# Kernel optimization log

Measured on AMD Instinct MI355X. Metric: run time of the kernel, lower is better.

## Reference

```python
import jax, jax.numpy as jnp
import numpy as np

B, T, N, F_IN = 8, 12, 20000, 2
H, HORIZON, K = 64, 12, 2
E = 320000


def setup_inputs() -> dict:
    key = jax.random.key(0)
    ks = jax.random.split(key, 12)
    s = 0.05
    return dict(
        x=jax.random.normal(ks[0], (B, T, N, F_IN), jnp.float32),
        edge_index=jax.random.randint(ks[1], (2, E), 0, N),
        edge_weight=jax.random.uniform(ks[2], (E,), jnp.float32),
        enc_w=jax.random.normal(ks[3], (F_IN, H), jnp.float32) * s,
        enc_b=jnp.zeros((H,), jnp.float32),
        node_emb=jax.random.normal(ks[4], (N, H), jnp.float32) * s,
        w_ih=jax.random.normal(ks[5], (3 * H, H), jnp.float32) * s,
        w_hh=jax.random.normal(ks[6], (3 * H, H), jnp.float32) * s,
        b_ih=jnp.zeros((3 * H,), jnp.float32),
        b_hh=jnp.zeros((3 * H,), jnp.float32),
        filt_w=jax.random.normal(ks[7], (H * (2 * K + 1), H), jnp.float32) * s,
        filt_b=jnp.zeros((H,), jnp.float32),
        dec_w=jax.random.normal(ks[8], (H, F_IN * HORIZON), jnp.float32) * s,
        dec_b=jnp.zeros((F_IN * HORIZON,), jnp.float32),
    )


def _gru_last(x_seq, w_ih, w_hh, b_ih, b_hh):
    # x_seq: [BN, T, H] -> last hidden state [BN, H] (torch GRU gate math)
    bn = x_seq.shape[0]
    h0 = jnp.zeros((bn, H), x_seq.dtype)
    # precompute input-side gates: [T, BN, 3H]
    xg = jnp.swapaxes(jnp.einsum('bth,gh->btg', x_seq, w_ih) + b_ih, 0, 1)

    def step(h, xg_t):
        hg = h @ w_hh.T + b_hh
        xr, xz, xn = jnp.split(xg_t, 3, axis=-1)
        hr, hz, hn = jnp.split(hg, 3, axis=-1)
        r = jax.nn.sigmoid(xr + hr)
        z = jax.nn.sigmoid(xz + hz)
        n = jnp.tanh(xn + r * hn)
        return (1.0 - z) * n + z * h, None

    h_last, _ = jax.lax.scan(step, h0, xg)
    return h_last


def _norm_weights(w, idx):
    # normalize edge weights by in-degree of aggregation index (tsl normalize)
    deg = jax.ops.segment_sum(w, idx, num_segments=N)
    inv = jnp.where(deg > 0, 1.0 / deg, 0.0)
    return w * inv[idx]


def _propagate(h, src, tgt, w):
    # h: [B, N, H]; message x_j * w aggregated (sum) at target
    msg = h[:, src, :] * w[None, :, None]           # [B, E, H]
    return jnp.zeros_like(h).at[:, tgt, :].add(msg)


def reference(x, edge_index, edge_weight, enc_w, enc_b, node_emb,
              w_ih, w_hh, b_ih, b_hh, filt_w, filt_b, dec_w, dec_b):
    b, t, n, _ = x.shape
    # linear encode + node embeddings
    x_emb = x @ enc_w + enc_b + node_emb[None, None]          # [B, T, N, H]
    # per-node GRU over time
    x_rnn = jnp.transpose(x_emb, (0, 2, 1, 3)).reshape(b * n, t, H)
    h = _gru_last(x_rnn, w_ih, w_hh, b_ih, b_hh).reshape(b, n, H)
    # diffusion graph conv: root + k hops forward + k hops backward
    src, tgt = edge_index[0], edge_index[1]
    w_fwd = _norm_weights(edge_weight, tgt)
    w_bwd = _norm_weights(edge_weight, src)
    outs = [h]
    for s_idx, t_idx, w in ((src, tgt, w_fwd), (tgt, src, w_bwd)):
        hs = h
        for _ in range(K):
            hs = _propagate(hs, s_idx, t_idx, w)
            outs.append(hs)
    z = jnp.concatenate(outs, axis=-1) @ filt_w + filt_b      # [B, N, H]
    # decode and rearrange 'b n (t f) -> b t n f'
    x_out = z @ dec_w + dec_b                                 # [B, N, HORIZON*F_IN]
    x_hor = x_out.reshape(b, n, HORIZON, F_IN)
    return jnp.transpose(x_hor, (0, 2, 1, 3))                 # [B, HORIZON, N, F_IN]
```

## Files before the change

kernel.cpp:

```cpp
#include <hip/hip_runtime.h>

#define NN 20000
#define NE 320000
#define NB 8
#define NT 12

typedef unsigned int u32;
typedef short bf16x8 __attribute__((ext_vector_type(8)));
typedef float f32x4 __attribute__((ext_vector_type(4)));
typedef u32   u32x2 __attribute__((ext_vector_type(2)));

union U8 { u32 u[4]; bf16x8 v; };

__device__ __forceinline__ float bcast(float v, int k) {
  return __int_as_float(__builtin_amdgcn_readlane(__float_as_int(v), k));
}
__device__ __forceinline__ u32 cvt_pk_bf16(float a, float b) {
  u32 r;
  asm("v_cvt_pk_bf16_f32 %0, %1, %2" : "=v"(r) : "v"(a), "v"(b));
  return r;
}
__device__ __forceinline__ float rcpf(float x) {
  float r;
  asm("v_rcp_f32 %0, %1" : "=v"(r) : "v"(x));
  return r;
}
__device__ __forceinline__ unsigned short f2bf(float f) {
  u32 u = __float_as_uint(f);
  u32 r = (u + 0x7FFFu + ((u >> 16) & 1u)) >> 16;
  return (unsigned short)r;
}
__device__ __forceinline__ float bf2f(unsigned short s) {
  return __uint_as_float(((u32)s) << 16);
}

__global__ void deg_kernel(const int* __restrict__ ei, const float* __restrict__ ew,
                           float* __restrict__ wsum_f, float* __restrict__ wsum_b,
                           int* __restrict__ cnt_f, int* __restrict__ cnt_b) {
  int e = blockIdx.x * 256 + threadIdx.x;
  if (e >= NE) return;
  int s = ei[e], t = ei[NE + e];
  float wv = ew[e];
  atomicAdd(&wsum_f[t], wv);
  atomicAdd(&cnt_f[t], 1);
  atomicAdd(&wsum_b[s], wv);
  atomicAdd(&cnt_b[s], 1);
}

__global__ __launch_bounds__(1024) void scan_kernel(
    const int* __restrict__ cnt_f, const int* __restrict__ cnt_b,
    int* __restrict__ rp_f, int* __restrict__ rp_b,
    int* __restrict__ cur_f, int* __restrict__ cur_b) {
  __shared__ int sm[1024];
  const int tid = threadIdx.x;
  for (int pass = 0; pass < 2; ++pass) {
    const int* cnt = pass ? cnt_b : cnt_f;
    int* rp  = pass ? rp_b  : rp_f;
    int* cur = pass ? cur_b : cur_f;
    const int base = tid * 20;
    int4 c4[5];
    int s = 0;
    if (base < NN) {
      const int4* cp = (const int4*)(cnt + base);
#pragma unroll
      for (int j = 0; j < 5; j++) c4[j] = cp[j];
#pragma unroll
      for (int j = 0; j < 5; j++) s += c4[j].x + c4[j].y + c4[j].z + c4[j].w;
    }
    __syncthreads();
    sm[tid] = s;
    __syncthreads();
    for (int off = 1; off < 1024; off <<= 1) {
      int v = (tid >= off) ? sm[tid - off] : 0;
      __syncthreads();
      sm[tid] += v;
      __syncthreads();
    }
    if (base < NN) {
      int run = sm[tid] - s;
      int4* rp4  = (int4*)(rp + base);
      int4* cur4 = (int4*)(cur + base);
#pragma unroll
      for (int j = 0; j < 5; j++) {
        int4 o;
        o.x = run; run += c4[j].x;
        o.y = run; run += c4[j].y;
        o.z = run; run += c4[j].z;
        o.w = run; run += c4[j].w;
        rp4[j] = o;
        cur4[j] = o;
      }
    }
    if (tid == 1023) rp[NN] = sm[1023];
  }
}

__global__ void fill_kernel(const int* __restrict__ ei, const float* __restrict__ ew,
                            const float* __restrict__ wsum_f, const float* __restrict__ wsum_b,
                            int* __restrict__ cur_f, int* __restrict__ cur_b,
                            int* __restrict__ col_f, float* __restrict__ wn_f,
                            int* __restrict__ col_b, float* __restrict__ wn_b) {
  int e = blockIdx.x * 256 + threadIdx.x;
  if (e >= NE) return;
  int s = ei[e], t = ei[NE + e];
  float wv = ew[e];
  int slot = atomicAdd(&cur_f[t], 1);
  float w1 = wsum_f[t];
  col_f[slot] = s;
  wn_f[slot] = (w1 > 0.f) ? wv / w1 : 0.f;
  slot = atomicAdd(&cur_b[s], 1);
  float w2 = wsum_b[s];
  col_b[slot] = t;
  wn_b[slot] = (w2 > 0.f) ? wv / w2 : 0.f;
}

__global__ __launch_bounds__(512) void nb_kernel(
    const float* __restrict__ node_emb, const float* __restrict__ enc_b,
    const float* __restrict__ w_ih, const float* __restrict__ b_ih,
    const float* __restrict__ enc_w, const float* __restrict__ b_hh,
    const float* __restrict__ filt_w, const float* __restrict__ filt_b,
    const float* __restrict__ dec_w, const float* __restrict__ dec_b,
    float* __restrict__ nbq, float* __restrict__ W2,
    float* __restrict__ Wcat, float* __restrict__ cbv) {
  const int tid = threadIdx.x;
  if (blockIdx.x >= NN / 8) {
    int idx = (blockIdx.x - NN / 8) * 512 + tid;
    if (idx < 64 * 128) {
      int k = idx >> 7, j = idx & 127;
      float acc = 0.f;
      if (j < 120) {
        int wi = j / 24, jj = j - wi * 24;
        for (int c = 0; c < 64; c++)
          acc += filt_w[(wi * 64 + k) * 64 + c] * dec_w[c * 24 + jj];
      }
      Wcat[idx] = acc;
    } else if (idx < 64 * 128 + 24) {
      int jj = idx - 64 * 128;
      float acc = dec_b[jj];
      for (int c = 0; c < 64; c++) acc += filt_b[c] * dec_w[c * 24 + jj];
      cbv[jj] = acc;
    }
    return;
  }
  __shared__ float w3[64 * 64 * 4];
  for (int idx = tid; idx < 192 * 64; idx += 512) {
    int row = idx >> 6, k = idx & 63;
    w3[((k << 6) + (row & 63)) * 4 + (row >> 6)] = w_ih[idx];
  }
  __syncthreads();
  const int lane = tid & 63, wave = tid >> 6;
  const int n = blockIdx.x * 8 + wave;
  float ne = node_emb[n * 64 + lane] + enc_b[lane];
  float ar = b_ih[lane], az = b_ih[64 + lane], an = b_ih[128 + lane];
  const float4* w3v = (const float4*)w3;
#pragma unroll 16
  for (int k = 0; k < 64; k++) {
    float4 w = w3v[(k << 6) + lane];
    float nk = bcast(ne, k);
    ar = fmaf(w.x, nk, ar);
    az = fmaf(w.y, nk, az);
    an = fmaf(w.z, nk, an);
  }
  nbq[(((lane >> 2)) * NN + n) * 4 + (lane & 3)]      = ar + b_hh[lane];
  nbq[((16 + (lane >> 2)) * NN + n) * 4 + (lane & 3)] = az + b_hh[64 + lane];
  nbq[((32 + (lane >> 2)) * NN + n) * 4 + (lane & 3)] = an;
  if (blockIdx.x == 0 && tid < 384) {
    int f = tid / 192, g = tid - f * 192;
    float acc = 0.f;
    for (int k2 = 0; k2 < 64; k2++) acc += enc_w[f * 64 + k2] * w_ih[g * 64 + k2];
    W2[f * 192 + g] = acc;
  }
}

#define MFMA(acc, a, b) acc = __builtin_amdgcn_mfma_f32_16x16x32_bf16((a), (b), acc, 0, 0, 0)

__global__ __launch_bounds__(256) void gru_kernel(
    const float* __restrict__ x, const float* __restrict__ nbq,
    const float* __restrict__ W2, const float* __restrict__ b_hh,
    const float* __restrict__ w_hh, const float* __restrict__ Wcat,
    const float* __restrict__ cbv,
    float* __restrict__ G0, float* __restrict__ G1f, float* __restrict__ G2f,
    float* __restrict__ G1b, float* __restrict__ G2b) {
  __shared__ u32 lds[16384];
  const int tid = threadIdx.x;

  for (int e = tid; e < 6144; e += 256) {
    int gate = e >> 5, k2 = (e & 31) << 1;
    float w0 = w_hh[gate * 64 + k2];
    float w1 = w_hh[gate * 64 + k2 + 1];
    unsigned short h0 = f2bf(w0), h1 = f2bf(w1);
    unsigned short l0 = f2bf(w0 - bf2f(h0)), l1 = f2bf(w1 - bf2f(h1));
    int tile = gate >> 4, ks = k2 >> 5;
    int ln = (gate & 15) + (((k2 >> 3) & 3) << 4);
    int r = (k2 >> 1) & 3;
    int idx = ((tile * 2 + ks) << 8) + (ln << 2) + r;
    lds[idx]        = (u32)h0 | ((u32)h1 << 16);
    lds[6144 + idx] = (u32)l0 | ((u32)l1 << 16);
  }
  __syncthreads();

  const int lane = tid & 63, wave = tid >> 6;
  const int g = lane >> 4, sl = lane & 15;
  const int seq = blockIdx.x * 64 + wave * 16 + sl;
  const int bb = seq / NN;
  const int node = seq - bb * NN;
  const u32 hxbase = 12288 + wave * 1024 + sl * 64;
  const u32 xw = ((u32)(sl & 7)) << 2;

  u32 w2h[12], w2l[12];
#pragma unroll
  for (int tl = 0; tl < 12; tl++) {
    float w0 = W2[tl * 16 + sl], w1 = W2[192 + tl * 16 + sl];
    u32 ph = cvt_pk_bf16(w0, w1);
    float lo0 = w0 - __uint_as_float(ph << 16);
    float lo1 = w1 - __uint_as_float(ph & 0xffff0000u);
    u32 pl = cvt_pk_bf16(lo0, lo1);
    w2h[tl] = (lane < 16) ? ph : 0u;
    w2l[tl] = (lane < 16) ? pl : 0u;
  }

  f32x4 nbA[4], nbB[4], nbC[4], bhnv[4];
#pragma unroll
  for (int fb = 0; fb < 4; fb++) {
    nbA[fb]  = *(const f32x4*)(nbq + ((size_t)(fb * 4 + g) * NN + node) * 4);
    nbB[fb]  = *(const f32x4*)(nbq + ((size_t)(16 + fb * 4 + g) * NN + node) * 4);
    nbC[fb]  = *(const f32x4*)(nbq + ((size_t)(32 + fb * 4 + g) * NN + node) * 4);
    bhnv[fb] = *(const f32x4*)(b_hh + 128 + fb * 16 + g * 4);
  }

  f32x4 hreg[4];
#pragma unroll
  for (int fb = 0; fb < 4; fb++) hreg[fb] = (f32x4){0.f, 0.f, 0.f, 0.f};

  const float* xptr = x + ((size_t)(bb * NT) * NN + node) * 2;

#define LDW(tile, ks, part) (*(const bf16x8*)(lds + (part) * 6144 + (((tile) * 2 + (ks)) << 8) + (lane << 2)))

  bf16x8 hb0, hb1, lb0, lb1;

#pragma unroll 1
  for (int t = 0; t < NT; t++) {
    float2 xv = *(const float2*)(xptr + (size_t)t * (NN * 2));
    u32 xhw = cvt_pk_bf16(xv.x, xv.y);
    float xl0 = xv.x - __uint_as_float(xhw << 16);
    float xl1 = xv.y - __uint_as_float(xhw & 0xffff0000u);
    u32 xlw = cvt_pk_bf16(xl0, xl1);
    U8 xB;
    xB.u[0] = xhw; xB.u[1] = xlw; xB.u[2] = xhw; xB.u[3] = 0u;

    if (t) {
      hb0 = *(const bf16x8*)(lds + hxbase +      ((u32)(0  + g * 4) ^ xw));
      hb1 = *(const bf16x8*)(lds + hxbase +      ((u32)(16 + g * 4) ^ xw));
      lb0 = *(const bf16x8*)(lds + hxbase + 32 + ((u32)(0  + g * 4) ^ xw));
      lb1 = *(const bf16x8*)(lds + hxbase + 32 + ((u32)(16 + g * 4) ^ xw));
    }

#pragma unroll
    for (int fb = 0; fb < 4; fb++) {
      f32x4 aR = nbA[fb], aZ = nbB[fb], aXN = nbC[fb], aHN = bhnv[fb];
      if (t) {
        bf16x8 Ah0 = LDW(fb, 0, 0), Al0 = LDW(fb, 0, 1);
        bf16x8 Ah1 = LDW(fb, 1, 0), Al1 = LDW(fb, 1, 1);
        MFMA(aR, Ah0, hb0); MFMA(aR, Ah0, lb0); MFMA(aR, Al0, hb0);
        MFMA(aR, Ah1, hb1); MFMA(aR, Ah1, lb1); MFMA(aR, Al1, hb1);
        bf16x8 Bh0 = LDW(4 + fb, 0, 0), Bl0 = LDW(4 + fb, 0, 1);
        bf16x8 Bh1 = LDW(4 + fb, 1, 0), Bl1 = LDW(4 + fb, 1, 1);
        MFMA(aZ, Bh0, hb0); MFMA(aZ, Bh0, lb0); MFMA(aZ, Bl0, hb0);
        MFMA(aZ, Bh1, hb1); MFMA(aZ, Bh1, lb1); MFMA(aZ, Bl1, hb1);
        bf16x8 Ch0 = LDW(8 + fb, 0, 0), Cl0 = LDW(8 + fb, 0, 1);
        bf16x8 Ch1 = LDW(8 + fb, 1, 0), Cl1 = LDW(8 + fb, 1, 1);
        MFMA(aHN, Ch0, hb0); MFMA(aHN, Ch0, lb0); MFMA(aHN, Cl0, hb0);
        MFMA(aHN, Ch1, hb1); MFMA(aHN, Ch1, lb1); MFMA(aHN, Cl1, hb1);
      }
      U8 aW;
      aW.u[0] = w2h[fb];     aW.u[1] = w2h[fb];     aW.u[2] = w2l[fb];     aW.u[3] = 0u;
      MFMA(aR, aW.v, xB.v);
      aW.u[0] = w2h[4 + fb]; aW.u[1] = w2h[4 + fb]; aW.u[2] = w2l[4 + fb];
      MFMA(aZ, aW.v, xB.v);
      aW.u[0] = w2h[8 + fb]; aW.u[1] = w2h[8 + fb]; aW.u[2] = w2l[8 + fb];
      MFMA(aXN, aW.v, xB.v);

      float hv[4];
#pragma unroll
      for (int r = 0; r < 4; r++) {
        float rr = rcpf(1.f + __expf(-aR[r]));
        float zz = rcpf(1.f + __expf(-aZ[r]));
        float nv = fmaf(rr, aHN[r], aXN[r]);
        float th = fmaf(-2.f, rcpf(1.f + __expf(2.f * nv)), 1.f);
        float h2 = fmaf(zz, hreg[fb][r] - th, th);
        hreg[fb][r] = h2;
        hv[r] = h2;
      }
      u32 hiA = cvt_pk_bf16(hv[0], hv[1]);
      u32 hiB = cvt_pk_bf16(hv[2], hv[3]);
      float l0 = hv[0] - __uint_as_float(hiA << 16);
      float l1 = hv[1] - __uint_as_float(hiA & 0xffff0000u);
      float l2 = hv[2] - __uint_as_float(hiB << 16);
      float l3 = hv[3] - __uint_as_float(hiB & 0xffff0000u);
      u32 loA = cvt_pk_bf16(l0, l1);
      u32 loB = cvt_pk_bf16(l2, l3);
      u32 off = hxbase + ((u32)(fb * 8 + g * 2) ^ xw);
      *(u32x2*)(lds + off)      = (u32x2){hiA, hiB};
      *(u32x2*)(lds + off + 32) = (u32x2){loA, loB};
    }
  }

  __syncthreads();
  for (int e = tid; e < 4096; e += 256) {
    int j = e >> 5, k2 = (e & 31) << 1;
    float w0 = Wcat[k2 * 128 + j];
    float w1 = Wcat[(k2 + 1) * 128 + j];
    unsigned short h0 = f2bf(w0), h1 = f2bf(w1);
    unsigned short l0 = f2bf(w0 - bf2f(h0)), l1 = f2bf(w1 - bf2f(h1));
    int tile = j >> 4, ks = k2 >> 5;
    int ln = (j & 15) + (((k2 >> 3) & 3) << 4);
    int r = (k2 >> 1) & 3;
    int idx = ((tile * 2 + ks) << 8) + (ln << 2) + r;
    lds[idx]        = (u32)h0 | ((u32)h1 << 16);
    lds[4096 + idx] = (u32)l0 | ((u32)l1 << 16);
  }
  __syncthreads();
  hb0 = *(const bf16x8*)(lds + hxbase +      ((u32)(0  + g * 4) ^ xw));
  hb1 = *(const bf16x8*)(lds + hxbase +      ((u32)(16 + g * 4) ^ xw));
  lb0 = *(const bf16x8*)(lds + hxbase + 32 + ((u32)(0  + g * 4) ^ xw));
  lb1 = *(const bf16x8*)(lds + hxbase + 32 + ((u32)(16 + g * 4) ^ xw));

#define LDC(tile, ks, part) (*(const bf16x8*)(lds + (part) * 4096 + (((tile) * 2 + (ks)) << 8) + (lane << 2)))
#pragma unroll
  for (int tile = 0; tile < 8; tile++) {
    f32x4 acc = (f32x4){0.f, 0.f, 0.f, 0.f};
    bf16x8 Ah0 = LDC(tile, 0, 0), Al0 = LDC(tile, 0, 1);
    MFMA(acc, Ah0, hb0); MFMA(acc, Ah0, lb0); MFMA(acc, Al0, hb0);
    bf16x8 Ah1 = LDC(tile, 1, 0), Al1 = LDC(tile, 1, 1);
    MFMA(acc, Ah1, hb1); MFMA(acc, Ah1, lb1); MFMA(acc, Al1, hb1);
#pragma unroll
    for (int r = 0; r < 4; r++) {
      int j = tile * 16 + g * 4 + r;
      if (j < 120) {
        int wi = j / 24, jj = j - wi * 24;
        float val = acc[r];
        if (wi == 0) val += cbv[jj];
        float* gb = (wi == 0) ? G0 : (wi == 1) ? G1f : (wi == 2) ? G2f : (wi == 3) ? G1b : G2b;
        gb[((size_t)node * NB + bb) * 24 + jj] = val;
      }
    }
  }
}

__global__ __launch_bounds__(192) void hop1_kernel(
    float* __restrict__ G1f, const float* __restrict__ G2f,
    float* __restrict__ G1b, const float* __restrict__ G2b,
    const int* __restrict__ rp_f, const int* __restrict__ col_f, const float* __restrict__ wn_f,
    const int* __restrict__ rp_b, const int* __restrict__ col_b, const float* __restrict__ wn_b) {
  const int tid = threadIdx.x;
  int blk = blockIdx.x;
  const int* rp; const int* col; const float* wn; float* dst; const float* src;
  int n;
  if (blk < NN) { n = blk;      rp = rp_f; col = col_f; wn = wn_f; dst = G1f; src = G2f; }
  else          { n = blk - NN; rp = rp_b; col = col_b; wn = wn_b; dst = G1b; src = G2b; }
  const int e0 = rp[n], e1 = rp[n + 1];
  float acc = 0.f;
  for (int e = e0; e < e1; ++e)
    acc = fmaf(wn[e], src[(size_t)col[e] * 192 + tid], acc);
  dst[(size_t)n * 192 + tid] += acc;
}

__global__ __launch_bounds__(192) void hop2_kernel(
    float* __restrict__ G0, const float* __restrict__ G1f, const float* __restrict__ G1b,
    const int* __restrict__ rp_f, const int* __restrict__ col_f, const float* __restrict__ wn_f,
    const int* __restrict__ rp_b, const int* __restrict__ col_b, const float* __restrict__ wn_b) {
  const int tid = threadIdx.x;
  const int n = blockIdx.x;
  float acc = G0[(size_t)n * 192 + tid];
  int e0 = rp_f[n], e1 = rp_f[n + 1];
  for (int e = e0; e < e1; ++e)
    acc = fmaf(wn_f[e], G1f[(size_t)col_f[e] * 192 + tid], acc);
  e0 = rp_b[n]; e1 = rp_b[n + 1];
  for (int e = e0; e < e1; ++e)
    acc = fmaf(wn_b[e], G1b[(size_t)col_b[e] * 192 + tid], acc);
  G0[(size_t)n * 192 + tid] = acc;
}

__global__ __launch_bounds__(256) void reorder_kernel(const float* __restrict__ G0,
                                                      float* __restrict__ out) {
  __shared__ float tile[32 * 193];
  const int n0 = blockIdx.x * 32;
  const int tid = threadIdx.x;
  for (int idx = tid; idx < 6144; idx += 256) {
    int i = idx / 192, r = idx - i * 192;
    tile[i * 193 + r] = G0[(size_t)n0 * 192 + idx];
  }
  __syncthreads();
  for (int idx = tid; idx < 6144; idx += 256) {
    int b = idx / 768;
    int rem = idx - b * 768;
    int t = rem >> 6;
    int rem2 = rem & 63;
    int i = rem2 >> 1, f = rem2 & 1;
    out[(((size_t)b * NT + t) * NN + n0 + i) * 2 + f] = tile[i * 193 + b * 24 + t * 2 + f];
  }
}

extern "C" void kernel_launch(void* const* d_in, const int* in_sizes, int n_in,
                              void* d_out, int out_size, void* d_ws, size_t ws_size,
                              hipStream_t stream) {
  const float* x        = (const float*)d_in[0];
  const int*   ei       = (const int*)d_in[1];
  const float* ew       = (const float*)d_in[2];
  const float* enc_w    = (const float*)d_in[3];
  const float* enc_b    = (const float*)d_in[4];
  const float* node_emb = (const float*)d_in[5];
  const float* w_ih     = (const float*)d_in[6];
  const float* w_hh     = (const float*)d_in[7];
  const float* b_ih     = (const float*)d_in[8];
  const float* b_hh     = (const float*)d_in[9];
  const float* filt_w   = (const float*)d_in[10];
  const float* filt_b   = (const float*)d_in[11];
  const float* dec_w    = (const float*)d_in[12];
  const float* dec_b    = (const float*)d_in[13];
  float* out = (float*)d_out;

  char* p = (char*)d_ws;
  auto alloc = [&](size_t bytes) {
    char* r = p;
    p += (bytes + 255) & ~(size_t)255;
    return r;
  };
  const size_t BN24 = (size_t)NB * NN * 24;
  float* G0   = (float*)alloc(BN24 * 4);
  float* G1f  = (float*)alloc(BN24 * 4);
  float* G2f  = (float*)alloc(BN24 * 4);
  float* G1b  = (float*)alloc(BN24 * 4);
  float* G2b  = (float*)alloc(BN24 * 4);
  float* nbq  = (float*)alloc((size_t)NN * 192 * 4);
  int* rp_f   = (int*)alloc((NN + 1) * 4);
  int* rp_b   = (int*)alloc((NN + 1) * 4);
  char* zreg  = alloc(4 * NN * 4);
  float* wsum_f = (float*)zreg;
  float* wsum_b = wsum_f + NN;
  int*   cnt_f  = (int*)(wsum_b + NN);
  int*   cnt_b  = cnt_f + NN;
  int* cur_f  = (int*)alloc(NN * 4);
  int* cur_b  = (int*)alloc(NN * 4);
  int* col_f  = (int*)alloc((size_t)NE * 4);
  float* wn_f = (float*)alloc((size_t)NE * 4);
  int* col_b  = (int*)alloc((size_t)NE * 4);
  float* wn_b = (float*)alloc((size_t)NE * 4);
  float* Wcat = (float*)alloc(64 * 128 * 4);
  float* cbv  = (float*)alloc(32 * 4);
  float* W2   = (float*)alloc(384 * 4);

  hipMemsetAsync(zreg, 0, 4 * NN * 4, stream);
  deg_kernel<<<(NE + 255) / 256, 256, 0, stream>>>(ei, ew, wsum_f, wsum_b, cnt_f, cnt_b);
  scan_kernel<<<1, 1024, 0, stream>>>(cnt_f, cnt_b, rp_f, rp_b, cur_f, cur_b);
  fill_kernel<<<(NE + 255) / 256, 256, 0, stream>>>(ei, ew, wsum_f, wsum_b, cur_f, cur_b,
                                                    col_f, wn_f, col_b, wn_b);
  nb_kernel<<<NN / 8 + 17, 512, 0, stream>>>(node_emb, enc_b, w_ih, b_ih, enc_w, b_hh,
                                             filt_w, filt_b, dec_w, dec_b,
                                             nbq, W2, Wcat, cbv);
  gru_kernel<<<(NB * NN) / 64, 256, 0, stream>>>(x, nbq, W2, b_hh, w_hh, Wcat, cbv,
                                                 G0, G1f, G2f, G1b, G2b);
  hop1_kernel<<<2 * NN, 192, 0, stream>>>(G1f, G2f, G1b, G2b,
                                          rp_f, col_f, wn_f, rp_b, col_b, wn_b);
  hop2_kernel<<<NN, 192, 0, stream>>>(G0, G1f, G1b,
                                      rp_f, col_f, wn_f, rp_b, col_b, wn_b);
  reorder_kernel<<<NN / 32, 256, 0, stream>>>(G0, out);
}
```

Before: 663.2 us.

## Rebalance nb, GRU and hop kernels: fewer blocks, bigger GRU tiles, wave-per-node SpMM

nb_kernel now uses 313 blocks that each loop over 64 nodes, so the w_ih transpose into LDS is done once per 64 nodes instead of once per 8. gru_kernel doubles to 512 threads covering 128 sequences per block with dynamic LDS, spreading the w_hh and Wcat staging over more work. The hop kernels assign one wave per node with float4 gathers over 48 lanes instead of one 192-thread block per node, cutting block count and widening memory accesses. The costs are 16 idle lanes per wave in the hop kernels, and possible occupancy limits from the larger GRU blocks and their 80 KB of LDS.

```diff
diff --git a/kernel.cpp b/kernel.cpp
--- a/kernel.cpp
+++ b/kernel.cpp
@@ -114,6 +114,7 @@
   wn_b[slot] = (w2 > 0.f) ? wv / w2 : 0.f;
 }
 
+#define NBLK_NB 313
 __global__ __launch_bounds__(512) void nb_kernel(
     const float* __restrict__ node_emb, const float* __restrict__ enc_b,
     const float* __restrict__ w_ih, const float* __restrict__ b_ih,
@@ -123,8 +124,8 @@
     float* __restrict__ nbq, float* __restrict__ W2,
     float* __restrict__ Wcat, float* __restrict__ cbv) {
   const int tid = threadIdx.x;
-  if (blockIdx.x >= NN / 8) {
-    int idx = (blockIdx.x - NN / 8) * 512 + tid;
+  if (blockIdx.x >= NBLK_NB) {
+    int idx = (blockIdx.x - NBLK_NB) * 512 + tid;
     if (idx < 64 * 128) {
       int k = idx >> 7, j = idx & 127;
       float acc = 0.f;
@@ -149,21 +150,28 @@
   }
   __syncthreads();
   const int lane = tid & 63, wave = tid >> 6;
-  const int n = blockIdx.x * 8 + wave;
-  float ne = node_emb[n * 64 + lane] + enc_b[lane];
-  float ar = b_ih[lane], az = b_ih[64 + lane], an = b_ih[128 + lane];
   const float4* w3v = (const float4*)w3;
+  const float eb = enc_b[lane];
+  const float bir = b_ih[lane], biz = b_ih[64 + lane], bin_ = b_ih[128 + lane];
+  const float bhr = b_hh[lane], bhz = b_hh[64 + lane];
+#pragma unroll 1
+  for (int pass = 0; pass < 8; ++pass) {
+    const int n = blockIdx.x * 64 + pass * 8 + wave;
+    if (n >= NN) break;
+    float ne = node_emb[n * 64 + lane] + eb;
+    float ar = bir, az = biz, an = bin_;
 #pragma unroll 16
-  for (int k = 0; k < 64; k++) {
-    float4 w = w3v[(k << 6) + lane];
-    float nk = bcast(ne, k);
-    ar = fmaf(w.x, nk, ar);
-    az = fmaf(w.y, nk, az);
-    an = fmaf(w.z, nk, an);
-  }
-  nbq[(((lane >> 2)) * NN + n) * 4 + (lane & 3)]      = ar + b_hh[lane];
-  nbq[((16 + (lane >> 2)) * NN + n) * 4 + (lane & 3)] = az + b_hh[64 + lane];
-  nbq[((32 + (lane >> 2)) * NN + n) * 4 + (lane & 3)] = an;
+    for (int k = 0; k < 64; k++) {
+      float4 w = w3v[(k << 6) + lane];
+      float nk = bcast(ne, k);
+      ar = fmaf(w.x, nk, ar);
+      az = fmaf(w.y, nk, az);
+      an = fmaf(w.z, nk, an);
+    }
+    nbq[(((lane >> 2)) * NN + n) * 4 + (lane & 3)]      = ar + bhr;
+    nbq[((16 + (lane >> 2)) * NN + n) * 4 + (lane & 3)] = az + bhz;
+    nbq[((32 + (lane >> 2)) * NN + n) * 4 + (lane & 3)] = an;
+  }
   if (blockIdx.x == 0 && tid < 384) {
     int f = tid / 192, g = tid - f * 192;
     float acc = 0.f;
@@ -174,17 +182,17 @@
 
 #define MFMA(acc, a, b) acc = __builtin_amdgcn_mfma_f32_16x16x32_bf16((a), (b), acc, 0, 0, 0)
 
-__global__ __launch_bounds__(256) void gru_kernel(
+__global__ __launch_bounds__(512) void gru_kernel(
     const float* __restrict__ x, const float* __restrict__ nbq,
     const float* __restrict__ W2, const float* __restrict__ b_hh,
     const float* __restrict__ w_hh, const float* __restrict__ Wcat,
     const float* __restrict__ cbv,
     float* __restrict__ G0, float* __restrict__ G1f, float* __restrict__ G2f,
     float* __restrict__ G1b, float* __restrict__ G2b) {
-  __shared__ u32 lds[16384];
+  extern __shared__ u32 lds[];
   const int tid = threadIdx.x;
 
-  for (int e = tid; e < 6144; e += 256) {
+  for (int e = tid; e < 6144; e += 512) {
     int gate = e >> 5, k2 = (e & 31) << 1;
     float w0 = w_hh[gate * 64 + k2];
     float w1 = w_hh[gate * 64 + k2 + 1];
@@ -201,7 +209,7 @@
 
   const int lane = tid & 63, wave = tid >> 6;
   const int g = lane >> 4, sl = lane & 15;
-  const int seq = blockIdx.x * 64 + wave * 16 + sl;
+  const int seq = blockIdx.x * 128 + wave * 16 + sl;
   const int bb = seq / NN;
   const int node = seq - bb * NN;
   const u32 hxbase = 12288 + wave * 1024 + sl * 64;
@@ -306,7 +314,7 @@
   }
 
   __syncthreads();
-  for (int e = tid; e < 4096; e += 256) {
+  for (int e = tid; e < 4096; e += 512) {
     int j = e >> 5, k2 = (e & 31) << 1;
     float w0 = Wcat[k2 * 128 + j];
     float w1 = Wcat[(k2 + 1) * 128 + j];
@@ -347,38 +355,71 @@
   }
 }
 
-__global__ __launch_bounds__(192) void hop1_kernel(
+__global__ __launch_bounds__(256) void hop1_kernel(
     float* __restrict__ G1f, const float* __restrict__ G2f,
     float* __restrict__ G1b, const float* __restrict__ G2b,
     const int* __restrict__ rp_f, const int* __restrict__ col_f, const float* __restrict__ wn_f,
     const int* __restrict__ rp_b, const int* __restrict__ col_b, const float* __restrict__ wn_b) {
-  const int tid = threadIdx.x;
-  int blk = blockIdx.x;
-  const int* rp; const int* col; const float* wn; float* dst; const float* src;
-  int n;
-  if (blk < NN) { n = blk;      rp = rp_f; col = col_f; wn = wn_f; dst = G1f; src = G2f; }
-  else          { n = blk - NN; rp = rp_b; col = col_b; wn = wn_b; dst = G1b; src = G2b; }
+  const int wv = threadIdx.x >> 6;
+  const int lane = threadIdx.x & 63;
+  const int task = blockIdx.x * 4 + wv;
+  const int fwd = task < NN;
+  const int n = fwd ? task : task - NN;
+  const int* rp  = fwd ? rp_f : rp_b;
+  const int* col = fwd ? col_f : col_b;
+  const float* wn = fwd ? wn_f : wn_b;
+  const float4* src = (const float4*)(fwd ? G2f : G2b);
+  float4* dst = (float4*)(fwd ? G1f : G1b);
   const int e0 = rp[n], e1 = rp[n + 1];
-  float acc = 0.f;
-  for (int e = e0; e < e1; ++e)
-    acc = fmaf(wn[e], src[(size_t)col[e] * 192 + tid], acc);
-  dst[(size_t)n * 192 + tid] += acc;
-}
-
-__global__ __launch_bounds__(192) void hop2_kernel(
+  if (lane >= 48) return;
+  float4 acc = {0.f, 0.f, 0.f, 0.f};
+  for (int e = e0; e < e1; ++e) {
+    const int c = col[e];
+    const float w = wn[e];
+    float4 v = src[(size_t)c * 48 + lane];
+    acc.x = fmaf(w, v.x, acc.x);
+    acc.y = fmaf(w, v.y, acc.y);
+    acc.z = fmaf(w, v.z, acc.z);
+    acc.w = fmaf(w, v.w, acc.w);
+  }
+  float4 d = dst[(size_t)n * 48 + lane];
+  d.x += acc.x; d.y += acc.y; d.z += acc.z; d.w += acc.w;
+  dst[(size_t)n * 48 + lane] = d;
+}
+
+__global__ __launch_bounds__(256) void hop2_kernel(
     float* __restrict__ G0, const float* __restrict__ G1f, const float* __restrict__ G1b,
     const int* __restrict__ rp_f, const int* __restrict__ col_f, const float* __restrict__ wn_f,
     const int* __restrict__ rp_b, const int* __restrict__ col_b, const float* __restrict__ wn_b) {
-  const int tid = threadIdx.x;
-  const int n = blockIdx.x;
-  float acc = G0[(size_t)n * 192 + tid];
+  const int wv = threadIdx.x >> 6;
+  const int lane = threadIdx.x & 63;
+  const int n = blockIdx.x * 4 + wv;
+  if (lane >= 48) return;
+  const float4* s1 = (const float4*)G1f;
+  const float4* s2 = (const float4*)G1b;
+  float4* dst = (float4*)G0;
+  float4 acc = dst[(size_t)n * 48 + lane];
   int e0 = rp_f[n], e1 = rp_f[n + 1];
-  for (int e = e0; e < e1; ++e)
-    acc = fmaf(wn_f[e], G1f[(size_t)col_f[e] * 192 + tid], acc);
+  for (int e = e0; e < e1; ++e) {
+    const int c = col_f[e];
+    const float w = wn_f[e];
+    float4 v = s1[(size_t)c * 48 + lane];
+    acc.x = fmaf(w, v.x, acc.x);
+    acc.y = fmaf(w, v.y, acc.y);
+    acc.z = fmaf(w, v.z, acc.z);
+    acc.w = fmaf(w, v.w, acc.w);
+  }
   e0 = rp_b[n]; e1 = rp_b[n + 1];
-  for (int e = e0; e < e1; ++e)
-    acc = fmaf(wn_b[e], G1b[(size_t)col_b[e] * 192 + tid], acc);
-  G0[(size_t)n * 192 + tid] = acc;
+  for (int e = e0; e < e1; ++e) {
+    const int c = col_b[e];
+    const float w = wn_b[e];
+    float4 v = s2[(size_t)c * 48 + lane];
+    acc.x = fmaf(w, v.x, acc.x);
+    acc.y = fmaf(w, v.y, acc.y);
+    acc.z = fmaf(w, v.z, acc.z);
+    acc.w = fmaf(w, v.w, acc.w);
+  }
+  dst[(size_t)n * 48 + lane] = acc;
 }
 
 __global__ __launch_bounds__(256) void reorder_kernel(const float* __restrict__ G0,
@@ -455,14 +496,14 @@
   scan_kernel<<<1, 1024, 0, stream>>>(cnt_f, cnt_b, rp_f, rp_b, cur_f, cur_b);
   fill_kernel<<<(NE + 255) / 256, 256, 0, stream>>>(ei, ew, wsum_f, wsum_b, cur_f, cur_b,
                                                     col_f, wn_f, col_b, wn_b);
-  nb_kernel<<<NN / 8 + 17, 512, 0, stream>>>(node_emb, enc_b, w_ih, b_ih, enc_w, b_hh,
-                                             filt_w, filt_b, dec_w, dec_b,
-                                             nbq, W2, Wcat, cbv);
-  gru_kernel<<<(NB * NN) / 64, 256, 0, stream>>>(x, nbq, W2, b_hh, w_hh, Wcat, cbv,
-                                                 G0, G1f, G2f, G1b, G2b);
-  hop1_kernel<<<2 * NN, 192, 0, stream>>>(G1f, G2f, G1b, G2b,
+  nb_kernel<<<NBLK_NB + 17, 512, 0, stream>>>(node_emb, enc_b, w_ih, b_ih, enc_w, b_hh,
+                                              filt_w, filt_b, dec_w, dec_b,
+                                              nbq, W2, Wcat, cbv);
+  gru_kernel<<<(NB * NN) / 128, 512, 20480 * 4, stream>>>(x, nbq, W2, b_hh, w_hh, Wcat, cbv,
+                                                          G0, G1f, G2f, G1b, G2b);
+  hop1_kernel<<<2 * NN / 4, 256, 0, stream>>>(G1f, G2f, G1b, G2b,
+                                              rp_f, col_f, wn_f, rp_b, col_b, wn_b);
+  hop2_kernel<<<NN / 4, 256, 0, stream>>>(G0, G1f, G1b,
                                           rp_f, col_f, wn_f, rp_b, col_b, wn_b);
-  hop2_kernel<<<NN, 192, 0, stream>>>(G0, G1f, G1b,
-                                      rp_f, col_f, wn_f, rp_b, col_b, wn_b);
   reorder_kernel<<<NN / 32, 256, 0, stream>>>(G0, out);
 }
```

After: 750.0 us. 1.13x slower.
